# Performance work log

Measured on AMD Instinct MI355X. Metric: run time of the kernel, lower is better.

The kernel has to match this reference:

```python
import jax, jax.numpy as jnp
import numpy as np

BN_EPS = 1e-5
INTERP_EPS = 1e-8


def setup_inputs() -> dict:
    key = jax.random.key(0)
    ks = jax.random.split(key, 8)
    B, N, S, D1, D2 = 8, 8192, 2048, 128, 256
    C_in, C_mid, C_out = D1 + D2, 256, 256
    return {
        "xyz1": jax.random.normal(ks[0], (B, 3, N), dtype=jnp.float32),
        "xyz2": jax.random.normal(ks[1], (B, 3, S), dtype=jnp.float32),
        "points1": jax.random.normal(ks[2], (B, D1, N), dtype=jnp.float32),
        "points2": jax.random.normal(ks[3], (B, D2, S), dtype=jnp.float32),
        "W0": jax.random.normal(ks[4], (C_mid, C_in), dtype=jnp.float32) * (1.0 / np.sqrt(C_in)),
        "b0": jnp.zeros((C_mid,), dtype=jnp.float32),
        "gamma0": jnp.ones((C_mid,), dtype=jnp.float32),
        "beta0": jnp.zeros((C_mid,), dtype=jnp.float32),
        "W1": jax.random.normal(ks[5], (C_out, C_mid), dtype=jnp.float32) * (1.0 / np.sqrt(C_mid)),
        "b1": jnp.zeros((C_out,), dtype=jnp.float32),
    }


def reference(xyz1, xyz2, points1, points2, W0, b0, gamma0, beta0, W1, b1):
    B, _, N = xyz1.shape
    S = xyz2.shape[2]
    x1 = jnp.transpose(xyz1, (0, 2, 1))  # (B, N, 3)
    x2 = jnpp = jnp.transpose(xyz2, (0, 2, 1))  # (B, S, 3)
    # squared distances: (B, N, S)
    d = (jnp.sum(x1 ** 2, -1)[:, :, None]
         + jnp.sum(x2 ** 2, -1)[:, None, :]
         - 2.0 * jnp.einsum('bnc,bsc->bns', x1, x2))
    # 3 nearest neighbors (fused top-3 instead of full sort; same math)
    neg_d, idx = jax.lax.top_k(-d, 3)  # (B, N, 3)
    dists = -neg_d
    recip = 1.0 / (dists + INTERP_EPS)
    weight = recip / jnp.sum(recip, axis=2, keepdims=True)  # (B, N, 3)
    p2t = jnp.transpose(points2, (0, 2, 1))  # (B, S, D2)
    D2 = p2t.shape[-1]
    gathered = jnp.take_along_axis(p2t, idx.reshape(B, N * 3, 1), axis=1).reshape(B, N, 3, D2)
    interp = jnp.einsum('bnkc,bnk->bcn', gathered, weight)  # (B, D2, N)
    new_points = jnp.concatenate([interp, points1], axis=1)  # (B, D2+D1, N)
    # conv0 (1x1) + BatchNorm (train mode, batch stats) + ReLU
    h = jnp.einsum('oc,bcn->bon', W0, new_points) + b0[None, :, None]
    mean = jnp.mean(h, axis=(0, 2), keepdims=True)
    var = jnp.mean((h - mean) ** 2, axis=(0, 2), keepdims=True)  # biased, as torch BN
    h = gamma0[None, :, None] * (h - mean) * jax.lax.rsqrt(var + BN_EPS) + beta0[None, :, None]
    h = jax.nn.relu(h)
    # conv1 (1x1) + Identity (module pairs conv1 with nn.Identity) + ReLU
    h = jnp.einsum('oc,bcn->bon', W1, h) + b1[None, :, None]
    return jax.nn.relu(h)
```

## Files before the change

### kernel.cpp

```cpp
#include <hip/hip_runtime.h>
#include <stdint.h>

constexpr int B = 8, N = 8192, S = 2048, D1 = 128, D2 = 256;
constexpr int CIN = 384, CMID = 256, COUT = 256;

typedef __attribute__((ext_vector_type(8))) _Float16 half8;
typedef __attribute__((ext_vector_type(4))) _Float16 half4;
typedef __attribute__((ext_vector_type(4))) float f32x4;

union HU { uint32_t u; _Float16 h[2]; };


__global__ __launch_bounds__(256) void k_top3(const float* __restrict__ xyz1,
                                              const float* __restrict__ xyz2,
                                              uint32_t* __restrict__ pw3) {
  __shared__ float4 Pq[S];
  __shared__ float md[4][3][64];
  __shared__ int mi[4][3][64];
  __shared__ float snrm[64];
  const int tid = threadIdx.x;
  const int wv = tid >> 6, lane = tid & 63;
  const int b = blockIdx.y;
  const int n = blockIdx.x * 64 + lane;
  const float* x1 = xyz1 + (size_t)b * 3 * N;
  const float ax = x1[n], ay = x1[n + N], az = x1[n + 2 * N];
  const float* x2 = xyz2 + (size_t)b * 3 * S;

  for (int j = tid; j < S; j += 256) {
    float sx = x2[j], sy = x2[j + S], sz = x2[j + 2 * S];
    Pq[j] = float4{sx, sy, sz, sx * sx + sy * sy + sz * sz};
  }
  if (wv == 0) snrm[lane] = ax * ax + ay * ay + az * az;
  __syncthreads();

  const float nax = -2.f * ax, nay = -2.f * ay, naz = -2.f * az;
  float e0 = 1e30f, e1 = 1e30f, e2 = 1e30f;
  int j0 = 0, j1 = 0, j2 = 0;
  const int s0 = wv * (S / 4), s1 = s0 + (S / 4);
#pragma unroll 8
  for (int s = s0; s < s1; ++s) {
    const float4 v = Pq[s];
    const float d = fmaf(nax, v.x, fmaf(nay, v.y, fmaf(naz, v.z, v.w)));
    const bool c0 = d < e0, c1 = d < e1, c2 = d < e2;
    const int t2 = c1 ? j1 : s;
    const int t1 = c0 ? j0 : s;
    j2 = c2 ? t2 : j2;
    j1 = c1 ? t1 : j1;
    j0 = c0 ? s : j0;
    e2 = __builtin_amdgcn_fmed3f(e1, e2, d);
    e1 = __builtin_amdgcn_fmed3f(e0, e1, d);
    e0 = fminf(e0, d);
  }
  md[wv][0][lane] = e0; mi[wv][0][lane] = j0;
  md[wv][1][lane] = e1; mi[wv][1][lane] = j1;
  md[wv][2][lane] = e2; mi[wv][2][lane] = j2;
  __syncthreads();
  if (tid < 64) {
    float f0 = md[0][0][tid], f1 = md[0][1][tid], f2 = md[0][2][tid];
    int g0 = mi[0][0][tid], g1 = mi[0][1][tid], g2 = mi[0][2][tid];
#pragma unroll
    for (int w = 1; w < 4; ++w)
#pragma unroll
      for (int k = 0; k < 3; ++k) {
        float d = md[w][k][tid];
        int i = mi[w][k][tid];
        if (d < f2) {
          if (d < f1) {
            f2 = f1; g2 = g1;
            if (d < f0) { f1 = f0; g1 = g0; f0 = d; g0 = i; }
            else        { f1 = d;  g1 = i; }
          } else { f2 = d; g2 = i; }
        }
      }
    const float rn = snrm[tid];
    float q0 = fmaxf(f0 + rn, 0.f);
    float q1 = fmaxf(f1 + rn, 0.f);
    float q2 = fmaxf(f2 + rn, 0.f);
    float r0 = 1.0f / (q0 + 1e-8f), r1 = 1.0f / (q1 + 1e-8f), r2 = 1.0f / (q2 + 1e-8f);
    float inv = 1.0f / (r0 + r1 + r2);
    auto pack = [](int i, float w) -> uint32_t {
      uint32_t q = (uint32_t)(w * 2097152.0f + 0.5f);
      if (q > 0x1FFFFFu) q = 0x1FFFFFu;
      return ((uint32_t)i << 21) | q;
    };
    size_t base = ((size_t)b * N + blockIdx.x * 64 + tid) * 3;
    pw3[base]     = pack(g0, r0 * inv);
    pw3[base + 1] = pack(g1, r1 * inv);
    pw3[base + 2] = pack(g2, r2 * inv);
  }
}

__global__ __launch_bounds__(256) void k_G(const float* __restrict__ points2,
                                           const float* __restrict__ W0,
                                           float* __restrict__ dout) {
  __shared__ half8 A_lds[4][256];
  __shared__ half8 B_lds[4][32];
  __shared__ float CT[32][258];
  const int tid = threadIdx.x;
  const int b = blockIdx.x >> 6;
  const int s0 = (blockIdx.x & 63) * 32;
  f32x4 acc[4][2] = {};
  const int wv = tid >> 6, lane = tid & 63;
  const int ln = lane & 15, quad = lane >> 4;
  const int bn = tid & 31, bkc = tid >> 5;
  const int ar = tid >> 3, ac4 = tid & 7;

  for (int kk = 0; kk < 256; kk += 32) {
    __syncthreads();
#pragma unroll
    for (int p = 0; p < 8; ++p) {
      int row = ar + 32 * p;
      const float4 v = *(const float4*)(W0 + (size_t)row * CIN + kk + ac4 * 4);
      half4 hv = {(_Float16)v.x, (_Float16)v.y, (_Float16)v.z, (_Float16)v.w};
      *(half4*)((_Float16*)&A_lds[ac4 >> 1][row] + (ac4 & 1) * 4) = hv;
    }
    {
      half4 hv;
#pragma unroll
      for (int j = 0; j < 4; ++j)
        hv[j] = (_Float16)points2[((size_t)(b * 256 + kk + bkc * 4 + j)) * S + s0 + bn];
      *(half4*)((_Float16*)&B_lds[bkc >> 1][bn] + (bkc & 1) * 4) = hv;
    }
    __syncthreads();
    half8 af[4], bf[2];
#pragma unroll
    for (int i = 0; i < 4; ++i) af[i] = A_lds[quad][wv * 64 + i * 16 + ln];
#pragma unroll
    for (int j = 0; j < 2; ++j) bf[j] = B_lds[quad][j * 16 + ln];
#pragma unroll
    for (int i = 0; i < 4; ++i)
#pragma unroll
      for (int j = 0; j < 2; ++j)
        acc[i][j] = __builtin_amdgcn_mfma_f32_16x16x32_f16(af[i], bf[j], acc[i][j], 0, 0, 0);
  }
  __syncthreads();
#pragma unroll
  for (int i = 0; i < 4; ++i)
#pragma unroll
    for (int reg = 0; reg < 4; ++reg) {
      int row = wv * 64 + i * 16 + quad * 4 + reg;
#pragma unroll
      for (int j = 0; j < 2; ++j) CT[j * 16 + ln][row] = acc[i][j][reg];
    }
  __syncthreads();
  const int sl = tid >> 3, g = tid & 7;
  float* g0 = dout + ((size_t)(b * 256 + 128)) * 8192 + (size_t)(s0 + sl) * 256 + g * 32;
#pragma unroll
  for (int q = 0; q < 8; ++q)
    *(float4*)(g0 + q * 4) = *(const float4*)&CT[sl][g * 32 + q * 4];
}

__global__ __launch_bounds__(256) void k_interp(const uint32_t* __restrict__ pw3,
                                                const float* __restrict__ dout_c,
                                                uint32_t* __restrict__ dout_u) {
  __shared__ int sidx[96];
  __shared__ float sw[96];
  const int tid = threadIdx.x;
  const int b = blockIdx.x >> 8;
  const int n0 = (blockIdx.x & 255) * 32;
  if (tid < 96) {
    uint32_t p = pw3[((size_t)b * N + n0) * 3 + tid];
    sidx[tid] = (int)(p >> 21);
    sw[tid] = (float)(p & 0x1FFFFFu) * (1.0f / 2097152.0f);
  }
  __syncthreads();
  const int colL = tid >> 3, p = tid & 7;
  const float* Gb = dout_c + ((size_t)(b * 256 + 128)) * 8192;
  float a[32];
#pragma unroll
  for (int q = 0; q < 32; ++q) a[q] = 0.f;
#pragma unroll
  for (int k = 0; k < 3; ++k) {
    int j = sidx[colL * 3 + k];
    float w = sw[colL * 3 + k];
    const float* g = Gb + (size_t)j * 256 + p * 32;
#pragma unroll
    for (int q = 0; q < 8; ++q) {
      float4 v = *(const float4*)(g + q * 4);
      a[q * 4 + 0] += w * v.x; a[q * 4 + 1] += w * v.y;
      a[q * 4 + 2] += w * v.z; a[q * 4 + 3] += w * v.w;
    }
  }
#pragma unroll
  for (int q = 0; q < 16; ++q) {
    int cp = p * 16 + q;
    HU u;
    u.h[0] = (_Float16)a[2 * q];
    u.h[1] = (_Float16)a[2 * q + 1];
    dout_u[((size_t)(b * 256 + cp)) * 8192 + n0 + colL] = u.u;
  }
}

__global__ __launch_bounds__(256) void k_h(uint32_t* __restrict__ h2,
                                           float* __restrict__ dpart,
                                           const float* __restrict__ points1,
                                           const float* __restrict__ W0,
                                           const float* __restrict__ b0) {
  __shared__ half8 A_lds[4][256];
  __shared__ half8 B_lds[4][64];
  __shared__ float red_s[256], red_q[256], sb0[256];
  const int tid = threadIdx.x;
  const int b = blockIdx.x >> 7;
  const int cb = blockIdx.x & 127;
  const int n0 = cb * 64;
  sb0[tid] = b0[tid];
  f32x4 acc[4][4] = {};
  const int wv = tid >> 6, lane = tid & 63;
  const int ln = lane & 15, quad = lane >> 4;
  const int bn = tid & 63, bkc = tid >> 6;
  const int ar = tid >> 3, ac4 = tid & 7;

  for (int kk = 0; kk < 128; kk += 32) {
    __syncthreads();
#pragma unroll
    for (int p = 0; p < 8; ++p) {
      int row = ar + 32 * p;
      const float4 v = *(const float4*)(W0 + (size_t)row * CIN + 256 + kk + ac4 * 4);
      half4 hv = {(_Float16)v.x, (_Float16)v.y, (_Float16)v.z, (_Float16)v.w};
      *(half4*)((_Float16*)&A_lds[ac4 >> 1][row] + (ac4 & 1) * 4) = hv;
    }
    {
      half8 hv;
#pragma unroll
      for (int j = 0; j < 8; ++j)
        hv[j] = (_Float16)points1[((size_t)(b * D1 + kk + bkc * 8 + j)) * N + n0 + bn];
      B_lds[bkc][bn] = hv;
    }
    __syncthreads();
    half8 af[4], bf[4];
#pragma unroll
    for (int i = 0; i < 4; ++i) af[i] = A_lds[quad][wv * 64 + i * 16 + ln];
#pragma unroll
    for (int j = 0; j < 4; ++j) bf[j] = B_lds[quad][j * 16 + ln];
#pragma unroll
    for (int i = 0; i < 4; ++i)
#pragma unroll
      for (int j = 0; j < 4; ++j)
        acc[i][j] = __builtin_amdgcn_mfma_f32_16x16x32_f16(af[i], bf[j], acc[i][j], 0, 0, 0);
  }
#pragma unroll
  for (int i = 0; i < 4; ++i) {
    const int rb = wv * 64 + i * 16 + quad * 4;
    const int cp0 = rb >> 1;
    float rs[4] = {0.f, 0.f, 0.f, 0.f}, rq[4] = {0.f, 0.f, 0.f, 0.f};
#pragma unroll
    for (int jj = 0; jj < 4; ++jj) {
      const int col = n0 + jj * 16 + ln;
      size_t a0 = ((size_t)(b * 256 + cp0)) * 8192 + col;
      HU ua, ub;
      ua.u = h2[a0];
      ub.u = h2[a0 + 8192];
      _Float16 e0 = (_Float16)(acc[i][jj][0] + (float)ua.h[0] + sb0[rb + 0]);
      _Float16 e1 = (_Float16)(acc[i][jj][1] + (float)ua.h[1] + sb0[rb + 1]);
      _Float16 e2 = (_Float16)(acc[i][jj][2] + (float)ub.h[0] + sb0[rb + 2]);
      _Float16 e3 = (_Float16)(acc[i][jj][3] + (float)ub.h[1] + sb0[rb + 3]);
      HU o0, o1;
      o0.h[0] = e0; o0.h[1] = e1; o1.h[0] = e2; o1.h[1] = e3;
      h2[a0] = o0.u;
      h2[a0 + 8192] = o1.u;
      float f0 = (float)e0, f1 = (float)e1, f2 = (float)e2, f3 = (float)e3;
      rs[0] += f0; rq[0] += f0 * f0;
      rs[1] += f1; rq[1] += f1 * f1;
      rs[2] += f2; rq[2] += f2 * f2;
      rs[3] += f3; rq[3] += f3 * f3;
    }
#pragma unroll
    for (int reg = 0; reg < 4; ++reg) {
      float s = rs[reg], q = rq[reg];
#pragma unroll
      for (int m = 1; m < 16; m <<= 1) {
        s += __shfl_xor(s, m);
        q += __shfl_xor(q, m);
      }
      if (ln == 0) { red_s[rb + reg] = s; red_q[rb + reg] = q; }
    }
  }
  __syncthreads();
  float* part = dpart + ((size_t)(b * 256 + 192)) * 8192 + (size_t)cb * 512;
  part[tid] = red_s[tid];
  part[256 + tid] = red_q[tid];
}

__global__ __launch_bounds__(256) void k_bn(const float* __restrict__ dpart,
                                            const float* __restrict__ gamma,
                                            const float* __restrict__ beta,
                                            float* __restrict__ bna,
                                            float* __restrict__ bnb) {
  const int c = blockIdx.x;
  const int tid = threadIdx.x;
  float s = 0.f, q = 0.f;
#pragma unroll
  for (int u = tid; u < 1024; u += 256) {
    int b = u >> 7, cb = u & 127;
    const float* part = dpart + ((size_t)(b * 256 + 192)) * 8192 + (size_t)cb * 512;
    s += part[c];
    q += part[256 + c];
  }
#pragma unroll
  for (int m = 1; m < 64; m <<= 1) {
    s += __shfl_xor(s, m);
    q += __shfl_xor(q, m);
  }
  __shared__ float ls[4], lq[4];
  if ((tid & 63) == 0) { ls[tid >> 6] = s; lq[tid >> 6] = q; }
  __syncthreads();
  if (tid == 0) {
    float st = ls[0] + ls[1] + ls[2] + ls[3];
    float qt = lq[0] + lq[1] + lq[2] + lq[3];
    const float invn = 1.0f / (float)(B * N);
    float mean = st * invn;
    float var = qt * invn - mean * mean;
    float a = gamma[c] * rsqrtf(var + 1e-5f);
    bna[c] = a;
    bnb[c] = beta[c] - mean * a;
  }
}

__global__ __launch_bounds__(256) void k_fused1(const uint32_t* h2,
                                                const float* __restrict__ W1,
                                                const float* __restrict__ b1,
                                                const float* __restrict__ bna,
                                                const float* __restrict__ bnb,
                                                float* out) {
  __shared__ uint32_t Hh[32 * 65 * 4];
  __shared__ float sa[256], sb[256], sb1[256];
  const int tid = threadIdx.x;
  const int b = blockIdx.x >> 7;
  const int n0 = (blockIdx.x & 127) * 64;
  sa[tid] = bna[tid]; sb[tid] = bnb[tid]; sb1[tid] = b1[tid];
  __syncthreads();
  {
    const int col = tid & 63, cpb = tid >> 6;
#pragma unroll
    for (int q = 0; q < 32; ++q) {
      int cp = cpb * 32 + q;
      HU u;
      u.u = h2[((size_t)(b * 256 + cp)) * 8192 + n0 + col];
      int k0 = 2 * cp;
      float v0 = sa[k0] * (float)u.h[0] + sb[k0];
      float v1 = sa[k0 + 1] * (float)u.h[1] + sb[k0 + 1];
      HU o;
      o.h[0] = (_Float16)(v0 > 0.f ? v0 : 0.f);
      o.h[1] = (_Float16)(v1 > 0.f ? v1 : 0.f);
      Hh[((cp >> 2) * 65 + col) * 4 + (cp & 3)] = o.u;
    }
  }
  __syncthreads();
  f32x4 acc[4][4] = {};
  const int wv = tid >> 6, lane = tid & 63;
  const int ln = lane & 15, quad = lane >> 4;
  for (int kk = 0; kk < 256; kk += 32) {
    half8 af[4], bf[4];
#pragma unroll
    for (int i = 0; i < 4; ++i) {
      int row = wv * 64 + i * 16 + ln;
      const float* wr = W1 + (size_t)row * CMID + kk + quad * 8;
      float4 w0 = *(const float4*)wr;
      float4 w1v = *(const float4*)(wr + 4);
      af[i] = half8{(_Float16)w0.x, (_Float16)w0.y, (_Float16)w0.z, (_Float16)w0.w,
                    (_Float16)w1v.x, (_Float16)w1v.y, (_Float16)w1v.z, (_Float16)w1v.w};
    }
#pragma unroll
    for (int j = 0; j < 4; ++j)
      bf[j] = *(const half8*)&Hh[(((kk >> 3) + quad) * 65 + j * 16 + ln) * 4];
#pragma unroll
    for (int i = 0; i < 4; ++i)
#pragma unroll
      for (int j = 0; j < 4; ++j)
        acc[i][j] = __builtin_amdgcn_mfma_f32_16x16x32_f16(af[i], bf[j], acc[i][j], 0, 0, 0);
  }
#pragma unroll
  for (int i = 0; i < 4; ++i) {
    const int rb = wv * 64 + i * 16 + quad * 4;
#pragma unroll
    for (int reg = 0; reg < 4; ++reg) {
      int row = rb + reg;
      float bias = sb1[row];
      float* orow = out + ((size_t)(b * 256 + row)) * 8192 + n0;
#pragma unroll
      for (int j = 0; j < 4; ++j)
        orow[j * 16 + ln] = fmaxf(acc[i][j][reg] + bias, 0.f);
    }
  }
}

extern "C" void kernel_launch(void* const* d_in, const int* in_sizes, int n_in,
                              void* d_out, int out_size, void* d_ws, size_t ws_size,
                              hipStream_t stream) {
  const float* xyz1 = (const float*)d_in[0];
  const float* xyz2 = (const float*)d_in[1];
  const float* points1 = (const float*)d_in[2];
  const float* points2 = (const float*)d_in[3];
  const float* W0 = (const float*)d_in[4];
  const float* b0 = (const float*)d_in[5];
  const float* gamma0 = (const float*)d_in[6];
  const float* beta0 = (const float*)d_in[7];
  const float* W1 = (const float*)d_in[8];
  const float* b1 = (const float*)d_in[9];
  float* out = (float*)d_out;

  char* ws = (char*)d_ws;
  float* bna = (float*)ws;
  float* bnb = (float*)(ws + 1024);
  uint32_t* pw3 = (uint32_t*)(ws + 2048);

  k_top3<<<dim3(N / 64, B), 256, 0, stream>>>(xyz1, xyz2, pw3);
  k_G<<<dim3(B * 64), 256, 0, stream>>>(points2, W0, out);
  k_interp<<<dim3(B * N / 32), 256, 0, stream>>>(pw3, out, (uint32_t*)out);
  k_h<<<dim3(B * N / 64), 256, 0, stream>>>((uint32_t*)out, out, points1, W0, b0);
  k_bn<<<dim3(256), 256, 0, stream>>>(out, gamma0, beta0, bna, bnb);
  k_fused1<<<dim3(B * N / 64), 256, 0, stream>>>((const uint32_t*)out, W1, b1,
                                                 bna, bnb, out);
}
```

Before: 341.5 us.

## Pre-convert W1 to fp16 and halve the conv1 column tile

Adds a small kernel that converts W1 to fp16 once into workspace, so the final conv1 kernel loads half8 fragments directly instead of converting fp32 weights on every tile. The final kernel now covers 32 columns per block instead of 64, which doubles the grid and halves the LDS tile. It also reads the BN'd hidden activations with 16-byte vector loads. The cost is more blocks that each re-read W1 with less reuse, plus one extra launch. W1h reuses the pw3 workspace slot, which is safe only because k_interp has finished with pw3 before the conversion kernel runs on the same stream.

```diff
diff --git a/kernel.cpp b/kernel.cpp
--- a/kernel.cpp
+++ b/kernel.cpp
@@ -191,6 +191,14 @@
   }
 }
 
+__global__ __launch_bounds__(256) void k_w1h(const float* __restrict__ W1,
+                                             _Float16* __restrict__ W1h) {
+  const int gid = blockIdx.x * 256 + threadIdx.x;
+  const float4 v = *(const float4*)(W1 + (size_t)gid * 4);
+  half4 h = {(_Float16)v.x, (_Float16)v.y, (_Float16)v.z, (_Float16)v.w};
+  *(half4*)(W1h + (size_t)gid * 4) = h;
+}
+
 __global__ __launch_bounds__(256) void k_h(uint32_t* __restrict__ h2,
                                            float* __restrict__ dpart,
                                            const float* __restrict__ points1,
@@ -317,56 +325,59 @@
 }
 
 __global__ __launch_bounds__(256) void k_fused1(const uint32_t* h2,
-                                                const float* __restrict__ W1,
+                                                const _Float16* __restrict__ W1h,
                                                 const float* __restrict__ b1,
                                                 const float* __restrict__ bna,
                                                 const float* __restrict__ bnb,
                                                 float* out) {
-  __shared__ uint32_t Hh[32 * 65 * 4];
+  __shared__ uint32_t Hh[32 * 33 * 4];
   __shared__ float sa[256], sb[256], sb1[256];
   const int tid = threadIdx.x;
-  const int b = blockIdx.x >> 7;
-  const int n0 = (blockIdx.x & 127) * 64;
+  const int b = blockIdx.x >> 8;
+  const int n0 = (blockIdx.x & 255) * 32;
   sa[tid] = bna[tid]; sb[tid] = bnb[tid]; sb1[tid] = b1[tid];
   __syncthreads();
   {
-    const int col = tid & 63, cpb = tid >> 6;
-#pragma unroll
-    for (int q = 0; q < 32; ++q) {
-      int cp = cpb * 32 + q;
-      HU u;
-      u.u = h2[((size_t)(b * 256 + cp)) * 8192 + n0 + col];
-      int k0 = 2 * cp;
-      float v0 = sa[k0] * (float)u.h[0] + sb[k0];
-      float v1 = sa[k0 + 1] * (float)u.h[1] + sb[k0 + 1];
-      HU o;
-      o.h[0] = (_Float16)(v0 > 0.f ? v0 : 0.f);
-      o.h[1] = (_Float16)(v1 > 0.f ? v1 : 0.f);
-      Hh[((cp >> 2) * 65 + col) * 4 + (cp & 3)] = o.u;
-    }
-  }
-  __syncthreads();
-  f32x4 acc[4][4] = {};
+    const int c4 = tid & 7;
+    const int rg = tid >> 3;
+#pragma unroll
+    for (int q = 0; q < 4; ++q) {
+      const int cp = rg + 32 * q;
+      const uint4 v = *(const uint4*)&h2[((size_t)(b * 256 + cp)) * 8192 + n0 + c4 * 4];
+      const int k0 = 2 * cp;
+      const float a0 = sa[k0], a1 = sa[k0 + 1], b0v = sb[k0], b1v = sb[k0 + 1];
+      const int kc = cp >> 2, sub = cp & 3;
+      const uint32_t vv[4] = {v.x, v.y, v.z, v.w};
+#pragma unroll
+      for (int m = 0; m < 4; ++m) {
+        HU u; u.u = vv[m];
+        float v0 = a0 * (float)u.h[0] + b0v;
+        float v1 = a1 * (float)u.h[1] + b1v;
+        HU o;
+        o.h[0] = (_Float16)(v0 > 0.f ? v0 : 0.f);
+        o.h[1] = (_Float16)(v1 > 0.f ? v1 : 0.f);
+        Hh[((kc * 33) + c4 * 4 + m) * 4 + sub] = o.u;
+      }
+    }
+  }
+  __syncthreads();
+  f32x4 acc[4][2] = {};
   const int wv = tid >> 6, lane = tid & 63;
   const int ln = lane & 15, quad = lane >> 4;
   for (int kk = 0; kk < 256; kk += 32) {
-    half8 af[4], bf[4];
+    half8 af[4], bf[2];
 #pragma unroll
     for (int i = 0; i < 4; ++i) {
       int row = wv * 64 + i * 16 + ln;
-      const float* wr = W1 + (size_t)row * CMID + kk + quad * 8;
-      float4 w0 = *(const float4*)wr;
-      float4 w1v = *(const float4*)(wr + 4);
-      af[i] = half8{(_Float16)w0.x, (_Float16)w0.y, (_Float16)w0.z, (_Float16)w0.w,
-                    (_Float16)w1v.x, (_Float16)w1v.y, (_Float16)w1v.z, (_Float16)w1v.w};
-    }
-#pragma unroll
-    for (int j = 0; j < 4; ++j)
-      bf[j] = *(const half8*)&Hh[(((kk >> 3) + quad) * 65 + j * 16 + ln) * 4];
+      af[i] = *(const half8*)(W1h + (size_t)row * CMID + kk + quad * 8);
+    }
+#pragma unroll
+    for (int j = 0; j < 2; ++j)
+      bf[j] = *(const half8*)&Hh[(((kk >> 3) + quad) * 33 + j * 16 + ln) * 4];
 #pragma unroll
     for (int i = 0; i < 4; ++i)
 #pragma unroll
-      for (int j = 0; j < 4; ++j)
+      for (int j = 0; j < 2; ++j)
         acc[i][j] = __builtin_amdgcn_mfma_f32_16x16x32_f16(af[i], bf[j], acc[i][j], 0, 0, 0);
   }
 #pragma unroll
@@ -378,7 +389,7 @@
       float bias = sb1[row];
       float* orow = out + ((size_t)(b * 256 + row)) * 8192 + n0;
 #pragma unroll
-      for (int j = 0; j < 4; ++j)
+      for (int j = 0; j < 2; ++j)
         orow[j * 16 + ln] = fmaxf(acc[i][j][reg] + bias, 0.f);
     }
   }
@@ -403,12 +414,14 @@
   float* bna = (float*)ws;
   float* bnb = (float*)(ws + 1024);
   uint32_t* pw3 = (uint32_t*)(ws + 2048);
+  _Float16* W1h = (_Float16*)(ws + 2048);
 
   k_top3<<<dim3(N / 64, B), 256, 0, stream>>>(xyz1, xyz2, pw3);
   k_G<<<dim3(B * 64), 256, 0, stream>>>(points2, W0, out);
   k_interp<<<dim3(B * N / 32), 256, 0, stream>>>(pw3, out, (uint32_t*)out);
+  k_w1h<<<dim3(64), 256, 0, stream>>>(W1, W1h);
   k_h<<<dim3(B * N / 64), 256, 0, stream>>>((uint32_t*)out, out, points1, W0, b0);
   k_bn<<<dim3(256), 256, 0, stream>>>(out, gamma0, beta0, bna, bnb);
-  k_fused1<<<dim3(B * N / 64), 256, 0, stream>>>((const uint32_t*)out, W1, b1,
+  k_fused1<<<dim3(B * N / 32), 256, 0, stream>>>((const uint32_t*)out, W1h, b1,
                                                  bna, bnb, out);
 }
```

New measurement: 320.5 us. 6.1% less time.
